# Optimization experiments

Measured on AMD Instinct MI355X. Metric: run time of the kernel, lower is better.

## Reference

```python
import jax, jax.numpy as jnp
import numpy as np

MB, K_LEN, Q_LEN = 8, 1024, 1024
D_IN, N_HEAD, OUT_DIM = 1024, 8, 1024
HID = D_IN // N_HEAD  # 128


def setup_inputs() -> dict:
    key = jax.random.key(0)
    ks = jax.random.split(key, 9)
    stdv = 1.0 / np.sqrt(HID)
    lin = 1.0 / np.sqrt(D_IN)
    return {
        "k": jax.random.normal(ks[0], (MB, K_LEN, D_IN), jnp.float32),
        "q": jax.random.normal(ks[1], (MB, Q_LEN, D_IN), jnp.float32),
        "Wk": jax.random.uniform(ks[2], (D_IN, N_HEAD * HID), jnp.float32, -lin, lin),
        "bk": jax.random.uniform(ks[3], (N_HEAD * HID,), jnp.float32, -lin, lin),
        "Wq": jax.random.uniform(ks[4], (D_IN, N_HEAD * HID), jnp.float32, -lin, lin),
        "bq": jax.random.uniform(ks[5], (N_HEAD * HID,), jnp.float32, -lin, lin),
        "w": jax.random.uniform(ks[6], (2 * HID,), jnp.float32, -stdv, stdv),
        "Wp": jax.random.uniform(ks[7], (N_HEAD * HID, OUT_DIM), jnp.float32, -lin, lin),
        "bp": jax.random.uniform(ks[8], (OUT_DIM,), jnp.float32, -lin, lin),
    }


def reference(k, q, Wk, bk, Wq, bq, w, Wp, bp):
    mb, k_len, _ = k.shape
    q_len = q.shape[1]
    # project and fold heads into the batch dim: (n_head*mb, len, hid)
    kx = (k @ Wk + bk).reshape(mb, k_len, N_HEAD, HID)
    kx = jnp.transpose(kx, (2, 0, 1, 3)).reshape(N_HEAD * mb, k_len, HID)
    qx = (q @ Wq + bq).reshape(mb, q_len, N_HEAD, HID)
    qx = jnp.transpose(qx, (2, 0, 1, 3)).reshape(N_HEAD * mb, q_len, HID)
    # additive (Bahdanau) score: matmul(cat(kxx, qxx), w) == kx@w_k + qx@w_q
    # (decomposition avoids the (hb, q_len, k_len, 2*hid) intermediate)
    ks_ = kx @ w[:HID]          # (hb, k_len)
    qs_ = qx @ w[HID:]          # (hb, q_len)
    score = jax.nn.softmax(jnp.tanh(qs_[:, :, None] + ks_[:, None, :]), axis=-1)
    out = jnp.einsum('bqk,bkh->bqh', score, kx)  # (hb, q_len, hid)
    # undo head folding: split dim0 into heads, concat on feature dim
    out = jnp.transpose(out.reshape(N_HEAD, mb, q_len, HID), (1, 2, 0, 3))
    out = out.reshape(mb, q_len, N_HEAD * HID)
    out = out @ Wp + bp  # dropout is identity in eval mode
    return out, score
```

## Files before the change

### kernel.cpp

```cpp
#include <hip/hip_runtime.h>
#include <math.h>

#define MB 8
#define NH 8
#define HID 128
#define SEQ 1024
#define DIN 1024
#define HBN 64

typedef __bf16 bf16x8 __attribute__((ext_vector_type(8)));
typedef __attribute__((ext_vector_type(4))) float f32x4;
typedef __attribute__((ext_vector_type(8))) unsigned short u16x8;
typedef __attribute__((ext_vector_type(4))) unsigned short u16x4;

__device__ inline unsigned short f2bf(float f) {
  unsigned int u = __builtin_bit_cast(unsigned int, f);
  u = (u + 0x7FFFu + ((u >> 16) & 1u)) >> 16;
  return (unsigned short)u;
}

__device__ inline float fast_expt(float x) {
  float e2 = __builtin_amdgcn_exp2f(x * 2.885390082f);
  float t = fmaf(-2.f, __builtin_amdgcn_rcpf(e2 + 1.f), 1.f);
  return __builtin_amdgcn_exp2f(t * 1.442695041f);
}

__device__ inline void gload_lds16(const void* g, void* l) {
  __builtin_amdgcn_global_load_lds(
      (const __attribute__((address_space(1))) void*)g,
      (__attribute__((address_space(3))) void*)l, 16, 0, 0);
}


__global__ __launch_bounds__(256) void cvt_bf16(const float* __restrict__ in,
                                                unsigned short* __restrict__ out) {
  const size_t idx = (size_t)blockIdx.x * 256 + threadIdx.x;
  const float4 v0 = *reinterpret_cast<const float4*>(in + idx * 8);
  const float4 v1 = *reinterpret_cast<const float4*>(in + idx * 8 + 4);
  u16x8 p;
  p[0] = f2bf(v0.x); p[1] = f2bf(v0.y); p[2] = f2bf(v0.z); p[3] = f2bf(v0.w);
  p[4] = f2bf(v1.x); p[5] = f2bf(v1.y); p[6] = f2bf(v1.z); p[7] = f2bf(v1.w);
  *reinterpret_cast<u16x8*>(out + idx * 8) = p;
}

__global__ __launch_bounds__(256) void transpose_bf16(const float* __restrict__ W,
                                                      unsigned short* __restrict__ WT) {
  __shared__ unsigned short tile[64][65];
  const int bx = blockIdx.x * 64;
  const int by = blockIdx.y * 64;
  const int tid = threadIdx.x;
  const int r = tid >> 4;
  const int c4 = tid & 15;
#pragma unroll
  for (int i = 0; i < 4; i++) {
    const int rr = r + i * 16;
    float4 v = *reinterpret_cast<const float4*>(W + (size_t)(bx + rr) * DIN + by + c4 * 4);
    tile[c4 * 4 + 0][rr] = f2bf(v.x);
    tile[c4 * 4 + 1][rr] = f2bf(v.y);
    tile[c4 * 4 + 2][rr] = f2bf(v.z);
    tile[c4 * 4 + 3][rr] = f2bf(v.w);
  }
  __syncthreads();
#pragma unroll
  for (int i = 0; i < 4; i++) {
    const int rr = r + i * 16;
    u16x4 o = {tile[rr][c4 * 4 + 0], tile[rr][c4 * 4 + 1],
               tile[rr][c4 * 4 + 2], tile[rr][c4 * 4 + 3]};
    *reinterpret_cast<u16x4*>(WT + (size_t)(by + rr) * DIN + bx + c4 * 4) = o;
  }
}

__global__ __launch_bounds__(256) void wq_fold(const float* __restrict__ Wq,
                                               const float* __restrict__ bq,
                                               const float* __restrict__ w,
                                               float* __restrict__ u) {
  const int tid = threadIdx.x;
  const int lane = tid & 63;
  const int wv = tid >> 6;
  const int row = blockIdx.x * 4 + wv;
  if (row > DIN) return;
  const int h = lane >> 3, sub = lane & 7;
  const float* src = (row < DIN) ? (Wq + (size_t)row * DIN) : bq;
  float p = 0.f;
  const int col0 = h * HID + sub * 16;
#pragma unroll
  for (int i = 0; i < 16; i++) p = fmaf(src[col0 + i], w[HID + sub * 16 + i], p);
  p += __shfl_xor(p, 1);
  p += __shfl_xor(p, 2);
  p += __shfl_xor(p, 4);
  if (sub == 0) u[(size_t)row * 8 + h] = p;
}

__global__ __launch_bounds__(256) void qs_kernel(const float* __restrict__ q,
                                                 const float* __restrict__ u,
                                                 float* __restrict__ qs) {
  __shared__ float ul[DIN * 9];
  __shared__ float cs[8];
  const int tid = threadIdx.x;
  for (int idx = tid; idx < DIN * 8; idx += 256)
    ul[(idx >> 3) * 9 + (idx & 7)] = u[idx];
  if (tid < 8) cs[tid] = u[DIN * 8 + tid];
  __syncthreads();
  const int lane = tid & 63, wv = tid >> 6;
  const int m = blockIdx.x * 4 + wv;
  const int b = m >> 10, t = m & 1023;
  float a0 = 0, a1 = 0, a2 = 0, a3 = 0, a4 = 0, a5 = 0, a6 = 0, a7 = 0;
  const float* qrow = q + (size_t)m * DIN;
#pragma unroll
  for (int i = 0; i < 16; i++) {
    const int din = lane + i * 64;
    const float v = qrow[din];
    const float* up = ul + din * 9;
    a0 = fmaf(v, up[0], a0); a1 = fmaf(v, up[1], a1);
    a2 = fmaf(v, up[2], a2); a3 = fmaf(v, up[3], a3);
    a4 = fmaf(v, up[4], a4); a5 = fmaf(v, up[5], a5);
    a6 = fmaf(v, up[6], a6); a7 = fmaf(v, up[7], a7);
  }
#pragma unroll
  for (int off = 1; off < 64; off <<= 1) {
    a0 += __shfl_xor(a0, off); a1 += __shfl_xor(a1, off);
    a2 += __shfl_xor(a2, off); a3 += __shfl_xor(a3, off);
    a4 += __shfl_xor(a4, off); a5 += __shfl_xor(a5, off);
    a6 += __shfl_xor(a6, off); a7 += __shfl_xor(a7, off);
  }
  if (lane == 0) {
    qs[((size_t)(0 * MB + b) << 10) + t] = a0 + cs[0];
    qs[((size_t)(1 * MB + b) << 10) + t] = a1 + cs[1];
    qs[((size_t)(2 * MB + b) << 10) + t] = a2 + cs[2];
    qs[((size_t)(3 * MB + b) << 10) + t] = a3 + cs[3];
    qs[((size_t)(4 * MB + b) << 10) + t] = a4 + cs[4];
    qs[((size_t)(5 * MB + b) << 10) + t] = a5 + cs[5];
    qs[((size_t)(6 * MB + b) << 10) + t] = a6 + cs[6];
    qs[((size_t)(7 * MB + b) << 10) + t] = a7 + cs[7];
  }
}

template <int MODE>
__global__ __launch_bounds__(256) void mfma_gemm(
    const unsigned short* __restrict__ A, const unsigned short* __restrict__ BT,
    const float* __restrict__ bias, const float* __restrict__ wseg,
    unsigned short* __restrict__ Cb, float* __restrict__ Cf,
    float* __restrict__ rowdot, int M, int N, int K) {
  __shared__ __align__(16) unsigned short Alds[128 * 32];
  __shared__ __align__(16) unsigned short Blds[128 * 32];

  const int tid = threadIdx.x;
  const int lane = tid & 63;
  const int wv = tid >> 6;
  const int g = lane >> 4;
  const int c = lane & 15;
  const int bm = blockIdx.y * 128;
  const int bn = blockIdx.x * 128;

  f32x4 acc[2][8];
#pragma unroll
  for (int m = 0; m < 2; m++)
#pragma unroll
    for (int n = 0; n < 8; n++) acc[m][n] = (f32x4){0.f, 0.f, 0.f, 0.f};

  for (int kt = 0; kt < K; kt += 32) {
#pragma unroll
    for (int i = 0; i < 2; i++) {
      const int cidx = i * 256 + tid;
      const int row = cidx >> 2;
      const int ko = (cidx & 3) << 3;
      if constexpr (MODE == 0) {
        gload_lds16(A + (size_t)(bm + row) * K + kt + ko, Alds + cidx * 8);
      } else {
        const int gr = bm + row;
        const int b = gr >> 10, t = gr & 1023;
        const int kk = kt + ko;
        const int h = kk >> 7, d = kk & 127;
        gload_lds16(A + (((size_t)(h * MB + b) * SEQ + t) << 7) + d,
                    Alds + cidx * 8);
      }
      gload_lds16(BT + (size_t)(bn + row) * K + kt + ko, Blds + cidx * 8);
    }
    __syncthreads();

    bf16x8 af[2], bfr[8];
#pragma unroll
    for (int m = 0; m < 2; m++)
      af[m] = *reinterpret_cast<const bf16x8*>(
          Alds + ((wv * 32 + m * 16 + c) * 32 + g * 8));
#pragma unroll
    for (int n = 0; n < 8; n++)
      bfr[n] = *reinterpret_cast<const bf16x8*>(Blds + ((n * 16 + c) * 32 + g * 8));
#pragma unroll
    for (int m = 0; m < 2; m++)
#pragma unroll
      for (int n = 0; n < 8; n++)
        acc[m][n] = __builtin_amdgcn_mfma_f32_16x16x32_bf16(af[m], bfr[n],
                                                            acc[m][n], 0, 0, 0);
    __syncthreads();
  }

  if constexpr (MODE == 0) {
    const int h = bn >> 7;
    const int b = bm >> 10;
    const size_t hb = h * MB + b;
    const int tbase = (bm & (SEQ - 1)) + wv * 32;
    float wl[8], bl[8];
#pragma unroll
    for (int n = 0; n < 8; n++) {
      wl[n] = wseg[n * 16 + c];
      bl[n] = bias[bn + n * 16 + c];
    }
#pragma unroll
    for (int m = 0; m < 2; m++) {
      const int t0 = tbase + m * 16 + g * 4;
      float pr0 = 0, pr1 = 0, pr2 = 0, pr3 = 0;
#pragma unroll
      for (int n = 0; n < 8; n++) {
        f32x4 a4 = acc[m][n];
        const float v0 = a4[0] + bl[n], v1 = a4[1] + bl[n];
        const float v2 = a4[2] + bl[n], v3 = a4[3] + bl[n];
        pr0 = fmaf(v0, wl[n], pr0); pr1 = fmaf(v1, wl[n], pr1);
        pr2 = fmaf(v2, wl[n], pr2); pr3 = fmaf(v3, wl[n], pr3);
        u16x4 o = {f2bf(v0), f2bf(v1), f2bf(v2), f2bf(v3)};
        *reinterpret_cast<u16x4*>(Cb + (hb * HID + n * 16 + c) * SEQ + t0) = o;
      }
#pragma unroll
      for (int off = 1; off < 16; off <<= 1) {
        pr0 += __shfl_xor(pr0, off); pr1 += __shfl_xor(pr1, off);
        pr2 += __shfl_xor(pr2, off); pr3 += __shfl_xor(pr3, off);
      }
      if (c == 0) {
        float* rd = rowdot + hb * SEQ + t0;
        rd[0] = pr0; rd[1] = pr1; rd[2] = pr2; rd[3] = pr3;
      }
    }
  } else {
#pragma unroll
    for (int m = 0; m < 2; m++) {
      const int r0 = bm + wv * 32 + m * 16 + g * 4;
#pragma unroll
      for (int n = 0; n < 8; n++) {
        f32x4 a4 = acc[m][n];
        const float bb = bias[bn + n * 16 + c];
#pragma unroll
        for (int r = 0; r < 4; r++)
          Cf[(size_t)(r0 + r) * N + bn + n * 16 + c] = a4[r] + bb;
      }
    }
  }
}

__global__ __launch_bounds__(256) void pv_fused(
    const unsigned short* __restrict__ kxT,
    const float* __restrict__ ks, const float* __restrict__ qs,
    float* __restrict__ score, unsigned short* __restrict__ att) {
  __shared__ __align__(16) unsigned short Alds[128 * 32];
  __shared__ __align__(16) unsigned short Blds[128 * 32];
  __shared__ __align__(16) float ksl[SEQ];
  __shared__ __align__(16) float qvl[128];
  __shared__ float invl[128];

  const int tid = threadIdx.x;
  const int hb = blockIdx.y;
  const int bm = blockIdx.x * 128;
  const int lane = tid & 63, wv = tid >> 6, g = lane >> 4, c = lane & 15;

  for (int i = tid; i < SEQ / 4; i += 256)
    *reinterpret_cast<float4*>(ksl + i * 4) =
        *reinterpret_cast<const float4*>(ks + ((size_t)hb << 10) + i * 4);
  if (tid < 32)
    *reinterpret_cast<float4*>(qvl + tid * 4) = *reinterpret_cast<const float4*>(
        qs + ((size_t)hb << 10) + bm + tid * 4);
  __syncthreads();

  {
    const int r = tid >> 1, h = tid & 1;
    const float qv = qvl[r];
    const float* kk = ksl + h * 512;
    float s0 = 0.f, s1 = 0.f;
    for (int i = 0; i < 512; i += 2) {
      s0 += fast_expt(qv + kk[i]);
      s1 += fast_expt(qv + kk[i + 1]);
    }
    float s = s0 + s1;
    s += __shfl_xor(s, 1);
    if (h == 0) invl[r] = __builtin_amdgcn_rcpf(s);
  }
  __syncthreads();

  f32x4 acc[2][8];
#pragma unroll
  for (int m = 0; m < 2; m++)
#pragma unroll
    for (int n = 0; n < 8; n++) acc[m][n] = (f32x4){0.f, 0.f, 0.f, 0.f};

  for (int kt = 0; kt < SEQ; kt += 32) {
#pragma unroll
    for (int i = 0; i < 2; i++) {
      const int cidx = i * 256 + tid;
      const int row = cidx >> 2;
      const int ko = (cidx & 3) << 3;
      gload_lds16(kxT + ((size_t)hb * HID + row) * SEQ + kt + ko, Blds + cidx * 8);
    }
#pragma unroll
    for (int i = 0; i < 2; i++) {
      const int cidx = i * 256 + tid;
      const int row = cidx >> 2;
      const int ko = (cidx & 3) << 3;
      const float qv = qvl[row];
      const float inv = invl[row];
      const float4 k0 = *reinterpret_cast<const float4*>(ksl + kt + ko);
      const float4 k1 = *reinterpret_cast<const float4*>(ksl + kt + ko + 4);
      const float p0 = fast_expt(qv + k0.x) * inv;
      const float p1 = fast_expt(qv + k0.y) * inv;
      const float p2 = fast_expt(qv + k0.z) * inv;
      const float p3 = fast_expt(qv + k0.w) * inv;
      const float p4 = fast_expt(qv + k1.x) * inv;
      const float p5 = fast_expt(qv + k1.y) * inv;
      const float p6 = fast_expt(qv + k1.z) * inv;
      const float p7 = fast_expt(qv + k1.w) * inv;
      float* sp = score + ((size_t)hb << 20) + ((size_t)(bm + row) << 10) + kt + ko;
      const float4 w0 = {p0, p1, p2, p3};
      const float4 w1 = {p4, p5, p6, p7};
      *reinterpret_cast<float4*>(sp) = w0;
      *reinterpret_cast<float4*>(sp + 4) = w1;
      bf16x8 pb;
      pb[0] = (__bf16)p0; pb[1] = (__bf16)p1; pb[2] = (__bf16)p2; pb[3] = (__bf16)p3;
      pb[4] = (__bf16)p4; pb[5] = (__bf16)p5; pb[6] = (__bf16)p6; pb[7] = (__bf16)p7;
      *reinterpret_cast<bf16x8*>(Alds + (size_t)cidx * 8) = pb;
    }
    __syncthreads();

    bf16x8 af[2], bfr[8];
#pragma unroll
    for (int m = 0; m < 2; m++)
      af[m] = *reinterpret_cast<const bf16x8*>(
          Alds + ((wv * 32 + m * 16 + c) * 32 + g * 8));
#pragma unroll
    for (int n = 0; n < 8; n++)
      bfr[n] = *reinterpret_cast<const bf16x8*>(Blds + ((n * 16 + c) * 32 + g * 8));
#pragma unroll
    for (int m = 0; m < 2; m++)
#pragma unroll
      for (int n = 0; n < 8; n++)
        acc[m][n] = __builtin_amdgcn_mfma_f32_16x16x32_bf16(af[m], bfr[n],
                                                            acc[m][n], 0, 0, 0);
    __syncthreads();
  }

#pragma unroll
  for (int m = 0; m < 2; m++) {
    const int q0 = bm + wv * 32 + m * 16 + g * 4;
#pragma unroll
    for (int n = 0; n < 8; n++) {
      f32x4 a4 = acc[m][n];
#pragma unroll
      for (int r = 0; r < 4; r++)
        att[((size_t)hb * SEQ + q0 + r) * HID + n * 16 + c] = f2bf(a4[r]);
    }
  }
}

extern "C" void kernel_launch(void* const* d_in, const int* in_sizes, int n_in,
                              void* d_out, int out_size, void* d_ws,
                              size_t ws_size, hipStream_t stream) {
  const float* k = (const float*)d_in[0];
  const float* q = (const float*)d_in[1];
  const float* Wk = (const float*)d_in[2];
  const float* bk = (const float*)d_in[3];
  const float* Wq = (const float*)d_in[4];
  const float* bq = (const float*)d_in[5];
  const float* w = (const float*)d_in[6];
  const float* Wp = (const float*)d_in[7];
  const float* bp = (const float*)d_in[8];

  float* out_ptr = (float*)d_out;
  float* score_ptr = out_ptr + (size_t)MB * SEQ * DIN;

  char* wsb = (char*)d_ws;
  unsigned short* kb = (unsigned short*)wsb;
  unsigned short* WkT = (unsigned short*)(wsb + 16777216);
  unsigned short* WpT = (unsigned short*)(wsb + 18874368);
  unsigned short* kxT = (unsigned short*)(wsb + 20971520);
  unsigned short* att = (unsigned short*)(wsb + 37748736);
  float* ks = (float*)(wsb + 54525952);
  float* qs = (float*)(wsb + 54788096);
  float* u = (float*)(wsb + 55050240);

  cvt_bf16<<<dim3(4096), dim3(256), 0, stream>>>(k, kb);
  transpose_bf16<<<dim3(16, 16), dim3(256), 0, stream>>>(Wk, WkT);
  transpose_bf16<<<dim3(16, 16), dim3(256), 0, stream>>>(Wp, WpT);
  wq_fold<<<dim3(257), dim3(256), 0, stream>>>(Wq, bq, w, u);
  qs_kernel<<<dim3(2048), dim3(256), 0, stream>>>(q, u, qs);
  mfma_gemm<0><<<dim3(8, 64), dim3(256), 0, stream>>>(
      kb, WkT, bk, w, kxT, nullptr, ks, MB * SEQ, DIN, DIN);
  pv_fused<<<dim3(8, HBN), dim3(256), 0, stream>>>(kxT, ks, qs, score_ptr, att);
  mfma_gemm<2><<<dim3(8, 64), dim3(256), 0, stream>>>(
      att, WpT, bp, nullptr, nullptr, out_ptr, nullptr, MB * SEQ, DIN, DIN);
}
```

Before: 200.8 us.

## Fuse k fp32-to-bf16 conversion into projection GEMM and merge prep kernels

Drops the standalone cvt_bf16 pass. The K-projection GEMM now loads fp32 k directly, converts it to bf16 and writes it to LDS, which avoids writing and re-reading a 16MB bf16 copy. The two weight transposes and the Wq fold are merged into one 3D-grid prep kernel, and the bias fold moves into qs_kernel, which cuts the launch count. Score and output stores become nontemporal. The cost is that the GEMM A-loads are now synchronous register loads rather than async global_load_lds, and each A tile is fetched at fp32 width, twice the bytes, once per N-block (8 times).

```diff
diff --git a/kernel.cpp b/kernel.cpp
--- a/kernel.cpp
+++ b/kernel.cpp
@@ -31,75 +31,77 @@
       (__attribute__((address_space(3))) void*)l, 16, 0, 0);
 }
 
-
-__global__ __launch_bounds__(256) void cvt_bf16(const float* __restrict__ in,
-                                                unsigned short* __restrict__ out) {
-  const size_t idx = (size_t)blockIdx.x * 256 + threadIdx.x;
-  const float4 v0 = *reinterpret_cast<const float4*>(in + idx * 8);
-  const float4 v1 = *reinterpret_cast<const float4*>(in + idx * 8 + 4);
-  u16x8 p;
-  p[0] = f2bf(v0.x); p[1] = f2bf(v0.y); p[2] = f2bf(v0.z); p[3] = f2bf(v0.w);
-  p[4] = f2bf(v1.x); p[5] = f2bf(v1.y); p[6] = f2bf(v1.z); p[7] = f2bf(v1.w);
-  *reinterpret_cast<u16x8*>(out + idx * 8) = p;
-}
-
-__global__ __launch_bounds__(256) void transpose_bf16(const float* __restrict__ W,
-                                                      unsigned short* __restrict__ WT) {
-  __shared__ unsigned short tile[64][65];
-  const int bx = blockIdx.x * 64;
-  const int by = blockIdx.y * 64;
+__global__ __launch_bounds__(256) void prep_kernel(
+    const float* __restrict__ Wk, const float* __restrict__ Wp,
+    const float* __restrict__ Wq, const float* __restrict__ w,
+    unsigned short* __restrict__ WkT, unsigned short* __restrict__ WpT,
+    float* __restrict__ u) {
+  const int z = blockIdx.z;
   const int tid = threadIdx.x;
-  const int r = tid >> 4;
-  const int c4 = tid & 15;
-#pragma unroll
-  for (int i = 0; i < 4; i++) {
-    const int rr = r + i * 16;
-    float4 v = *reinterpret_cast<const float4*>(W + (size_t)(bx + rr) * DIN + by + c4 * 4);
-    tile[c4 * 4 + 0][rr] = f2bf(v.x);
-    tile[c4 * 4 + 1][rr] = f2bf(v.y);
-    tile[c4 * 4 + 2][rr] = f2bf(v.z);
-    tile[c4 * 4 + 3][rr] = f2bf(v.w);
-  }
-  __syncthreads();
-#pragma unroll
-  for (int i = 0; i < 4; i++) {
-    const int rr = r + i * 16;
-    u16x4 o = {tile[rr][c4 * 4 + 0], tile[rr][c4 * 4 + 1],
-               tile[rr][c4 * 4 + 2], tile[rr][c4 * 4 + 3]};
-    *reinterpret_cast<u16x4*>(WT + (size_t)(by + rr) * DIN + bx + c4 * 4) = o;
-  }
-}
-
-__global__ __launch_bounds__(256) void wq_fold(const float* __restrict__ Wq,
-                                               const float* __restrict__ bq,
-                                               const float* __restrict__ w,
-                                               float* __restrict__ u) {
-  const int tid = threadIdx.x;
-  const int lane = tid & 63;
-  const int wv = tid >> 6;
-  const int row = blockIdx.x * 4 + wv;
-  if (row > DIN) return;
-  const int h = lane >> 3, sub = lane & 7;
-  const float* src = (row < DIN) ? (Wq + (size_t)row * DIN) : bq;
-  float p = 0.f;
-  const int col0 = h * HID + sub * 16;
-#pragma unroll
-  for (int i = 0; i < 16; i++) p = fmaf(src[col0 + i], w[HID + sub * 16 + i], p);
-  p += __shfl_xor(p, 1);
-  p += __shfl_xor(p, 2);
-  p += __shfl_xor(p, 4);
-  if (sub == 0) u[(size_t)row * 8 + h] = p;
+  if (z < 2) {
+    __shared__ unsigned short tile[64][65];
+    const float* W = (z == 0) ? Wk : Wp;
+    unsigned short* WT = (z == 0) ? WkT : WpT;
+    const int bx = blockIdx.x * 64;
+    const int by = blockIdx.y * 64;
+    const int r = tid >> 4;
+    const int c4 = tid & 15;
+#pragma unroll
+    for (int i = 0; i < 4; i++) {
+      const int rr = r + i * 16;
+      float4 v = *reinterpret_cast<const float4*>(W + (size_t)(bx + rr) * DIN + by + c4 * 4);
+      tile[c4 * 4 + 0][rr] = f2bf(v.x);
+      tile[c4 * 4 + 1][rr] = f2bf(v.y);
+      tile[c4 * 4 + 2][rr] = f2bf(v.z);
+      tile[c4 * 4 + 3][rr] = f2bf(v.w);
+    }
+    __syncthreads();
+#pragma unroll
+    for (int i = 0; i < 4; i++) {
+      const int rr = r + i * 16;
+      u16x4 o = {tile[rr][c4 * 4 + 0], tile[rr][c4 * 4 + 1],
+                 tile[rr][c4 * 4 + 2], tile[rr][c4 * 4 + 3]};
+      *reinterpret_cast<u16x4*>(WT + (size_t)(by + rr) * DIN + bx + c4 * 4) = o;
+    }
+  } else {
+    const int lane = tid & 63;
+    const int wv = tid >> 6;
+    const int bid = blockIdx.x + blockIdx.y * 16;
+    const int row = bid * 4 + wv;
+    const int h = lane >> 3, sub = lane & 7;
+    const float* src = Wq + (size_t)row * DIN;
+    float p = 0.f;
+    const int col0 = h * HID + sub * 16;
+#pragma unroll
+    for (int i = 0; i < 16; i++) p = fmaf(src[col0 + i], w[HID + sub * 16 + i], p);
+    p += __shfl_xor(p, 1);
+    p += __shfl_xor(p, 2);
+    p += __shfl_xor(p, 4);
+    if (sub == 0) u[(size_t)row * 8 + h] = p;
+  }
 }
 
 __global__ __launch_bounds__(256) void qs_kernel(const float* __restrict__ q,
                                                  const float* __restrict__ u,
+                                                 const float* __restrict__ bq,
+                                                 const float* __restrict__ w,
                                                  float* __restrict__ qs) {
   __shared__ float ul[DIN * 9];
   __shared__ float cs[8];
   const int tid = threadIdx.x;
   for (int idx = tid; idx < DIN * 8; idx += 256)
     ul[(idx >> 3) * 9 + (idx & 7)] = u[idx];
-  if (tid < 8) cs[tid] = u[DIN * 8 + tid];
+  if (tid < 64) {
+    const int h = tid >> 3, sub = tid & 7;
+    float p = 0.f;
+#pragma unroll
+    for (int i = 0; i < 16; i++)
+      p = fmaf(bq[h * HID + sub * 16 + i], w[HID + sub * 16 + i], p);
+    p += __shfl_xor(p, 1);
+    p += __shfl_xor(p, 2);
+    p += __shfl_xor(p, 4);
+    if (sub == 0) cs[h] = p;
+  }
   __syncthreads();
   const int lane = tid & 63, wv = tid >> 6;
   const int m = blockIdx.x * 4 + wv;
@@ -137,10 +139,10 @@
 
 template <int MODE>
 __global__ __launch_bounds__(256) void mfma_gemm(
-    const unsigned short* __restrict__ A, const unsigned short* __restrict__ BT,
-    const float* __restrict__ bias, const float* __restrict__ wseg,
-    unsigned short* __restrict__ Cb, float* __restrict__ Cf,
-    float* __restrict__ rowdot, int M, int N, int K) {
+    const unsigned short* __restrict__ A, const float* __restrict__ Af,
+    const unsigned short* __restrict__ BT, const float* __restrict__ bias,
+    const float* __restrict__ wseg, unsigned short* __restrict__ Cb,
+    float* __restrict__ Cf, float* __restrict__ rowdot, int M, int N, int K) {
   __shared__ __align__(16) unsigned short Alds[128 * 32];
   __shared__ __align__(16) unsigned short Blds[128 * 32];
 
@@ -165,7 +167,13 @@
       const int row = cidx >> 2;
       const int ko = (cidx & 3) << 3;
       if constexpr (MODE == 0) {
-        gload_lds16(A + (size_t)(bm + row) * K + kt + ko, Alds + cidx * 8);
+        const float* src = Af + (size_t)(bm + row) * K + kt + ko;
+        const float4 v0 = *reinterpret_cast<const float4*>(src);
+        const float4 v1 = *reinterpret_cast<const float4*>(src + 4);
+        u16x8 p;
+        p[0] = f2bf(v0.x); p[1] = f2bf(v0.y); p[2] = f2bf(v0.z); p[3] = f2bf(v0.w);
+        p[4] = f2bf(v1.x); p[5] = f2bf(v1.y); p[6] = f2bf(v1.z); p[7] = f2bf(v1.w);
+        *reinterpret_cast<u16x8*>(Alds + cidx * 8) = p;
       } else {
         const int gr = bm + row;
         const int b = gr >> 10, t = gr & 1023;
@@ -240,7 +248,8 @@
         const float bb = bias[bn + n * 16 + c];
 #pragma unroll
         for (int r = 0; r < 4; r++)
-          Cf[(size_t)(r0 + r) * N + bn + n * 16 + c] = a4[r] + bb;
+          __builtin_nontemporal_store(a4[r] + bb,
+                                      Cf + (size_t)(r0 + r) * N + bn + n * 16 + c);
       }
     }
   }
@@ -316,10 +325,10 @@
       const float p6 = fast_expt(qv + k1.z) * inv;
       const float p7 = fast_expt(qv + k1.w) * inv;
       float* sp = score + ((size_t)hb << 20) + ((size_t)(bm + row) << 10) + kt + ko;
-      const float4 w0 = {p0, p1, p2, p3};
-      const float4 w1 = {p4, p5, p6, p7};
-      *reinterpret_cast<float4*>(sp) = w0;
-      *reinterpret_cast<float4*>(sp + 4) = w1;
+      const f32x4 w0 = {p0, p1, p2, p3};
+      const f32x4 w1 = {p4, p5, p6, p7};
+      __builtin_nontemporal_store(w0, reinterpret_cast<f32x4*>(sp));
+      __builtin_nontemporal_store(w1, reinterpret_cast<f32x4*>(sp + 4));
       bf16x8 pb;
       pb[0] = (__bf16)p0; pb[1] = (__bf16)p1; pb[2] = (__bf16)p2; pb[3] = (__bf16)p3;
       pb[4] = (__bf16)p4; pb[5] = (__bf16)p5; pb[6] = (__bf16)p6; pb[7] = (__bf16)p7;
@@ -374,23 +383,21 @@
   float* score_ptr = out_ptr + (size_t)MB * SEQ * DIN;
 
   char* wsb = (char*)d_ws;
-  unsigned short* kb = (unsigned short*)wsb;
-  unsigned short* WkT = (unsigned short*)(wsb + 16777216);
-  unsigned short* WpT = (unsigned short*)(wsb + 18874368);
-  unsigned short* kxT = (unsigned short*)(wsb + 20971520);
-  unsigned short* att = (unsigned short*)(wsb + 37748736);
-  float* ks = (float*)(wsb + 54525952);
-  float* qs = (float*)(wsb + 54788096);
-  float* u = (float*)(wsb + 55050240);
-
-  cvt_bf16<<<dim3(4096), dim3(256), 0, stream>>>(k, kb);
-  transpose_bf16<<<dim3(16, 16), dim3(256), 0, stream>>>(Wk, WkT);
-  transpose_bf16<<<dim3(16, 16), dim3(256), 0, stream>>>(Wp, WpT);
-  wq_fold<<<dim3(257), dim3(256), 0, stream>>>(Wq, bq, w, u);
-  qs_kernel<<<dim3(2048), dim3(256), 0, stream>>>(q, u, qs);
+  unsigned short* WkT = (unsigned short*)(wsb);
+  unsigned short* WpT = (unsigned short*)(wsb + 2097152);
+  unsigned short* kxT = (unsigned short*)(wsb + 4194304);
+  unsigned short* att = (unsigned short*)(wsb + 20971520);
+  float* ks = (float*)(wsb + 37748736);
+  float* qs = (float*)(wsb + 38010880);
+  float* u = (float*)(wsb + 38273024);
+
+  prep_kernel<<<dim3(16, 16, 3), dim3(256), 0, stream>>>(Wk, Wp, Wq, w, WkT,
+                                                         WpT, u);
+  qs_kernel<<<dim3(2048), dim3(256), 0, stream>>>(q, u, bq, w, qs);
   mfma_gemm<0><<<dim3(8, 64), dim3(256), 0, stream>>>(
-      kb, WkT, bk, w, kxT, nullptr, ks, MB * SEQ, DIN, DIN);
+      nullptr, k, WkT, bk, w, kxT, nullptr, ks, MB * SEQ, DIN, DIN);
   pv_fused<<<dim3(8, HBN), dim3(256), 0, stream>>>(kxT, ks, qs, score_ptr, att);
   mfma_gemm<2><<<dim3(8, 64), dim3(256), 0, stream>>>(
-      att, WpT, bp, nullptr, nullptr, out_ptr, nullptr, MB * SEQ, DIN, DIN);
-}
+      att, nullptr, WpT, bp, nullptr, nullptr, out_ptr, nullptr, MB * SEQ, DIN,
+      DIN);
+}
```

Result: slower. 232.5 us (+15.7%).
